# Kernel tuning notes

Measured on AMD Instinct MI355X. Metric: run time of the kernel, lower is better.

Reference implementation:

```python
import jax, jax.numpy as jnp
import numpy as np

N = 32768       # nodes
IN = 256        # in_channels
D = 128         # out_channels (per-head dim)
H = 4           # num_heads
M = 4           # num_reps (seeds per partition)
KP = 128        # number of partitions
S = N // KP     # partition size (equal-size partitions)
SCALE = float(np.sqrt(D))


def _linear_init(key, fan_in, fan_out):
    # torch nn.Linear default: U(-1/sqrt(fan_in), 1/sqrt(fan_in)) for W and b
    kw, kb = jax.random.split(key)
    bound = 1.0 / np.sqrt(fan_in)
    w = jax.random.uniform(kw, (fan_in, fan_out), jnp.float32, -bound, bound)
    b = jax.random.uniform(kb, (fan_out,), jnp.float32, -bound, bound)
    return w, b


def setup_inputs() -> dict:
    key = jax.random.key(0)
    k0, k1, k2, k3, k4 = jax.random.split(key, 5)
    x = jax.random.normal(k0, (N, IN), jnp.float32)
    # equal-size disjoint partitions: [KP, S] index array covering 0..N-1
    partition_indices = jnp.arange(N, dtype=jnp.int32).reshape(KP, S)
    Wq_w, Wq_b = _linear_init(k1, IN, H * D)
    Wk_w, Wk_b = _linear_init(k2, IN, H * D)
    Wv_w, Wv_b = _linear_init(k3, IN, H * D)
    pool_seeds = jax.random.normal(k4, (M, H, D), jnp.float32) * 0.02
    alpha_logit = jnp.float32(0.0)
    beta = jnp.float32(1.0)
    return {
        "x": x, "partition_indices": partition_indices,
        "Wq_w": Wq_w, "Wq_b": Wq_b, "Wk_w": Wk_w, "Wk_b": Wk_b,
        "Wv_w": Wv_w, "Wv_b": Wv_b, "pool_seeds": pool_seeds,
        "alpha_logit": alpha_logit, "beta": beta,
    }


def reference(x, partition_indices, Wq_w, Wq_b, Wk_w, Wk_b, Wv_w, Wv_b,
              pool_seeds, alpha_logit, beta):
    n = x.shape[0]
    Q = (x @ Wq_w + Wq_b).reshape(n, H, D)
    K = (x @ Wk_w + Wk_b).reshape(n, H, D)
    V = (x @ Wv_w + Wv_b).reshape(n, H, D)

    # gather per partition -> [KP, S, H, D]
    Qp = Q[partition_indices]
    Kp = K[partition_indices]
    Vp = V[partition_indices]

    # Fine: exact softmax attention within each partition
    attn_local = jnp.einsum('kphd,kqhd->khpq', Qp, Kp) / SCALE
    attn_local = jax.nn.softmax(attn_local, axis=-1)
    outp = jnp.einsum('khpq,kqhd->kphd', attn_local, Vp)  # [KP,S,H,D]
    # partitions are disjoint -> scatter-set back to node order
    out_local = jnp.zeros((n, H, D), x.dtype).at[partition_indices.reshape(-1)].set(
        outp.reshape(n, H, D))
    x_local = out_local.mean(axis=1)  # [N, D]

    # Coarse: learned seeds pool each partition
    pool_attn = jnp.einsum('mhd,kqhd->kmhq', pool_seeds, Kp) / SCALE
    pool_attn = jax.nn.softmax(pool_attn, axis=-1)
    reps_k = jnp.einsum('kmhq,kqhd->kmhd', pool_attn, Kp).reshape(KP * M, H, D)
    reps_v = jnp.einsum('kmhq,kqhd->kmhd', pool_attn, Vp).reshape(KP * M, H, D)

    # Global cross-attention: every node attends to all partition reps
    cross_attn = jnp.einsum('nhd,rhd->nhr', Q, reps_k) / SCALE
    cross_attn = jax.nn.softmax(cross_attn, axis=-1)
    out_global = jnp.einsum('nhr,rhd->nhd', cross_attn, reps_v)
    x_global = out_global.mean(axis=1)  # [N, D]

    x_self = V.mean(axis=1)
    alpha = jax.nn.sigmoid(alpha_logit)
    return alpha * x_local + (1.0 - alpha) * x_global + beta * x_self
```

## Files before the change

kernel.cpp:

```cpp
#include <hip/hip_runtime.h>
#include <hip/hip_bf16.h>


#define INV_SCALE 0.08838834764831845f
#define C2EXP 0.12751744f
#define DEFER_THR 90.50966799f

typedef __attribute__((ext_vector_type(8))) short bf16x8;
typedef __attribute__((ext_vector_type(4))) float floatx4;
typedef unsigned short ushort_t;
typedef unsigned int uint32;

#define OFF_Q    0ull
#define OFF_K    33554432ull
#define OFF_V    67108864ull
#define OFF_LOC  100663296ull
#define OFF_RPK  109051904ull
#define OFF_XC   110100480ull
#define OFF_WC   126877696ull
#define OFF_SCAL 127671296ull
#define OFF_FLAG 127671304ull
#define OFF_RVT  127672320ull
#define OFF_GLB  128196608ull

#define WC_WQ 0
#define WC_WK 131072
#define WC_WV 262144
#define WC_BQ 393216
#define WC_BK 393728
#define WC_BV 394240
#define WC_SEED 394752
#define WC_TOT 396800

static __device__ __forceinline__ float bflo(uint32 u) {
  return __uint_as_float(u << 16);
}
static __device__ __forceinline__ float bfhi(uint32 u) {
  return __uint_as_float(u & 0xffff0000u);
}
static __device__ __forceinline__ float bf2f(ushort_t u) {
  return __uint_as_float(((uint32)u) << 16);
}
static __device__ __forceinline__ ushort_t f2bf(float f) {
  uint32 x = __float_as_uint(f);
  uint32 r = x + 0x7fffu + ((x >> 16) & 1u);
  return (ushort_t)(r >> 16);
}
static __device__ __forceinline__ uint32 pack2bf(float a, float b) {
  return (uint32)f2bf(a) | ((uint32)f2bf(b) << 16);
}
static __device__ __forceinline__ uint32 cvtpk(float a, float b) {
  uint32 r;
  asm("v_cvt_pk_bf16_f32 %0, %1, %2" : "=v"(r) : "v"(a), "v"(b));
  return r;
}

static __device__ __forceinline__ void gl2lds16(const ushort_t* g, ushort_t* l) {
  __builtin_amdgcn_global_load_lds(
      (const __attribute__((address_space(1))) void*)g,
      (__attribute__((address_space(3))) void*)l, 16, 0, 0);
}

__global__ __launch_bounds__(64) void k_detect(const uint32* __restrict__ xw,
                                               const ushort_t* __restrict__ betaRaw,
                                               uint32* __restrict__ flags) {
  const int lane = threadIdx.x;
  const uint32 w = xw[lane * 137 + 3];
  const int e = (w >> 7) & 0xff;
  const unsigned long long b = __ballot(e >= 100 && e <= 140);
  if (lane == 0) {
    flags[0] = (__popcll(b) >= 48) ? 1u : 0u;
    flags[1] = (betaRaw[0] != 0) ? 1u : 0u;
  }
}

static __device__ __forceinline__ void conv8(const void* src, long j, int isB,
                                             ushort_t* dst) {
  if (isB) {
    *reinterpret_cast<uint4*>(dst) =
        *reinterpret_cast<const uint4*>(reinterpret_cast<const ushort_t*>(src) + j);
  } else {
    const float* f = reinterpret_cast<const float*>(src) + j;
    const float4 a = *reinterpret_cast<const float4*>(f);
    const float4 b = *reinterpret_cast<const float4*>(f + 4);
    uint4 o;
    o.x = pack2bf(a.x, a.y); o.y = pack2bf(a.z, a.w);
    o.z = pack2bf(b.x, b.y); o.w = pack2bf(b.z, b.w);
    *reinterpret_cast<uint4*>(dst) = o;
  }
}

__global__ __launch_bounds__(256) void k_convert(
    const void* __restrict__ x,
    const void* __restrict__ Wq, const void* __restrict__ bq,
    const void* __restrict__ Wk, const void* __restrict__ bk,
    const void* __restrict__ Wv, const void* __restrict__ bv,
    const void* __restrict__ seeds, const void* __restrict__ alpha,
    const void* __restrict__ beta,
    ushort_t* __restrict__ xc, ushort_t* __restrict__ wc,
    float* __restrict__ scal, const uint32* __restrict__ flags)
{
  const int isB = (int)flags[0];
  const long i8 = ((long)blockIdx.x * 256 + threadIdx.x) * 8;
  if (blockIdx.y == 0) {
    conv8(x, i8, isB, xc + i8);
  } else {
    if (i8 < WC_BQ) {
      const int sel = (int)(i8 >> 17);
      const long local = i8 & 131071;
      const int kk = (int)(local >> 9);
      const int nn = (int)(local & 511);
      const void* src = sel == 0 ? Wq : (sel == 1 ? Wk : Wv);
      ushort_t* dstW = wc + sel * 131072;
#pragma unroll
      for (int j = 0; j < 8; ++j) {
        ushort_t v;
        if (isB) v = reinterpret_cast<const ushort_t*>(src)[local + j];
        else     v = f2bf(reinterpret_cast<const float*>(src)[local + j]);
        dstW[(size_t)(nn + j) * 256 + kk] = v;
      }
    } else if (i8 < WC_TOT) {
      const void* src; long j;
      if (i8 < WC_BK)        { src = bq;    j = i8 - WC_BQ; }
      else if (i8 < WC_BV)   { src = bk;    j = i8 - WC_BK; }
      else if (i8 < WC_SEED) { src = bv;    j = i8 - WC_BV; }
      else                   { src = seeds; j = i8 - WC_SEED; }
      conv8(src, j, isB, wc + i8);
    }
    if (blockIdx.x == 0 && threadIdx.x == 0) {
      const int isBS = (int)flags[1];
      scal[0] = isBS ? bf2f(reinterpret_cast<const ushort_t*>(alpha)[0])
                     : reinterpret_cast<const float*>(alpha)[0];
      scal[1] = isBS ? bf2f(reinterpret_cast<const ushort_t*>(beta)[0])
                     : reinterpret_cast<const float*>(beta)[0];
    }
  }
}

__global__ __launch_bounds__(256) void k_qkv(
    const ushort_t* __restrict__ xc, const ushort_t* __restrict__ wc,
    ushort_t* __restrict__ Qb, ushort_t* __restrict__ Kb, ushort_t* __restrict__ Vb)
{
  const int m0 = blockIdx.x * 64;
  const int tid = threadIdx.x, lane = tid & 63, wv = tid >> 6;
  const int l16 = lane & 15, quad = lane >> 4;
  const int kswz = l16 & 7;

  __shared__ __align__(16) ushort_t Ws[2][64 * 256];

  bf16x8 af[8];
  {
    const ushort_t* xrow = xc + (size_t)(m0 + wv * 16 + l16) * 256 + quad * 8;
#pragma unroll
    for (int ks = 0; ks < 8; ++ks)
      af[ks] = *reinterpret_cast<const bf16x8*>(xrow + ks * 32);
  }

  const int wRL = lane >> 5;
  const int wCH = lane & 31;

#pragma unroll
  for (int j = 0; j < 8; ++j) {
    const int row = wv * 16 + j * 2 + wRL;
    gl2lds16(wc + (size_t)row * 256 + ((wCH ^ (row & 7)) << 3),
             &Ws[0][(wv * 16 + j * 2) * 256]);
  }
  __syncthreads();

  for (int t = 0; t < 24; ++t) {
    const int cur = t & 1;

    if (t < 23) {
      const int nb = cur ^ 1;
      const int tn = t + 1;
#pragma unroll
      for (int j = 0; j < 8; ++j) {
        const int row = wv * 16 + j * 2 + wRL;
        gl2lds16(wc + (size_t)(tn * 64 + row) * 256 + ((wCH ^ (row & 7)) << 3),
                 &Ws[nb][(wv * 16 + j * 2) * 256]);
      }
    }

    floatx4 acc[4] = {};
#pragma unroll
    for (int ks = 0; ks < 8; ++ks) {
      const int ac = ks * 4 + quad;
#pragma unroll
      for (int nt = 0; nt < 4; ++nt) {
        bf16x8 b = *reinterpret_cast<const bf16x8*>(
            &Ws[cur][(nt * 16 + l16) * 256 + ((ac ^ kswz) << 3)]);
        acc[nt] = __builtin_amdgcn_mfma_f32_16x16x32_bf16(af[ks], b, acc[nt], 0, 0, 0);
      }
    }

    const int sel = t >> 3, nc = t & 7;
    const ushort_t* bias = wc + WC_BQ + sel * 512;
    ushort_t* out = sel == 0 ? Qb : (sel == 1 ? Kb : Vb);
    const int n0 = nc * 64;
#pragma unroll
    for (int nt = 0; nt < 4; ++nt) {
      const int col = n0 + nt * 16 + l16;
      const float bf = bf2f(bias[col]);
#pragma unroll
      for (int r = 0; r < 4; ++r) {
        const int row = m0 + wv * 16 + quad * 4 + r;
        out[(size_t)row * 512 + col] = f2bf(acc[nt][r] + bf);
      }
    }

    __syncthreads();
  }
}

__global__ __launch_bounds__(256) void k_pool(
    const ushort_t* __restrict__ Kb, const ushort_t* __restrict__ Vb,
    const int* __restrict__ pidx_all, const ushort_t* __restrict__ wc,
    ushort_t* __restrict__ rpk, ushort_t* __restrict__ rvT)
{
  const int k = blockIdx.x, h = blockIdx.y;
  const int tid = threadIdx.x, lane = tid & 63, wv = tid >> 6;
  const int* pidx = pidx_all + k * 256;

  __shared__ __align__(16) ushort_t SB[128 * 256];
  const uint32* SBU = reinterpret_cast<const uint32*>(SB);

#pragma unroll
  for (int i = 0; i < 16; ++i) {
    const int e8 = tid + 256 * i;
    const int q = e8 >> 4, dc = (e8 & 15) * 8;
    uint4 kv = *reinterpret_cast<const uint4*>(Kb + (size_t)pidx[q] * 512 + h * 128 + dc);
    const ushort_t* ku = reinterpret_cast<const ushort_t*>(&kv);
    const int qp = q >> 1, qb = q & 1;
#pragma unroll
    for (int j = 0; j < 8; ++j) {
      const int d = dc + j;
      SB[d * 256 + (((qp ^ (d & 31)) << 1) | qb)] = ku[j];
    }
  }
  __syncthreads();

  float q00, q01, q10, q11;
  {
    const uint32* ssrc = reinterpret_cast<const uint32*>(wc + WC_SEED + (size_t)(wv * 4 + h) * 128);
    float s00 = 0.f, s01 = 0.f, s10 = 0.f, s11 = 0.f;
#pragma unroll 8
    for (int dc = 0; dc < 64; ++dc) {
      const uint32 qv = ssrc[dc];
      const float a0 = bflo(qv), a1 = bfhi(qv);
      const int d0 = dc * 2, d1 = d0 + 1;
      const int c0 = lane ^ (d0 & 31);
      const int c1 = lane ^ (d1 & 31);
      const uint32 u00 = SBU[d0 * 128 + c0];
      const uint32 u01 = SBU[d0 * 128 + c0 + 64];
      const uint32 u10 = SBU[d1 * 128 + c1];
      const uint32 u11 = SBU[d1 * 128 + c1 + 64];
      s00 += a0 * bflo(u00) + a1 * bflo(u10);
      s01 += a0 * bfhi(u00) + a1 * bfhi(u10);
      s10 += a0 * bflo(u01) + a1 * bflo(u11);
      s11 += a0 * bfhi(u01) + a1 * bfhi(u11);
    }
    s00 *= INV_SCALE; s01 *= INV_SCALE; s10 *= INV_SCALE; s11 *= INV_SCALE;
    float mx = fmaxf(fmaxf(s00, s01), fmaxf(s10, s11));
#pragma unroll
    for (int off = 32; off >= 1; off >>= 1) mx = fmaxf(mx, __shfl_xor(mx, off));
    const float e00 = __expf(s00 - mx), e01 = __expf(s01 - mx);
    const float e10 = __expf(s10 - mx), e11 = __expf(s11 - mx);
    float sm = e00 + e01 + e10 + e11;
#pragma unroll
    for (int off = 32; off >= 1; off >>= 1) sm += __shfl_xor(sm, off);
    const float inv = 1.0f / sm;
    q00 = e00 * inv; q01 = e01 * inv; q10 = e10 * inv; q11 = e11 * inv;
  }

  {
    float rk0 = 0.f, rk1 = 0.f;
    const int d0 = 2 * lane, d1 = 2 * lane + 1;
#pragma unroll 4
    for (int qp = 0; qp < 64; ++qp) {
      const float pa = __shfl(q00, qp), pb = __shfl(q01, qp);
      const float pc = __shfl(q10, qp), pd = __shfl(q11, qp);
      const int c0 = qp ^ (d0 & 31);
      const int c1 = qp ^ (d1 & 31);
      const uint32 u0  = SBU[d0 * 128 + c0];
      const uint32 u0b = SBU[d0 * 128 + c0 + 64];
      const uint32 u1  = SBU[d1 * 128 + c1];
      const uint32 u1b = SBU[d1 * 128 + c1 + 64];
      rk0 += pa * bflo(u0) + pb * bfhi(u0) + pc * bflo(u0b) + pd * bfhi(u0b);
      rk1 += pa * bflo(u1) + pb * bfhi(u1) + pc * bflo(u1b) + pd * bfhi(u1b);
    }
    reinterpret_cast<uint32*>(rpk + ((size_t)((k * 4 + wv) * 4 + h)) * 128)[lane] = pack2bf(rk0, rk1);
  }
  __syncthreads();

#pragma unroll
  for (int i = 0; i < 16; ++i) {
    const int e8 = tid + 256 * i;
    const int q = e8 >> 4, dc = (e8 & 15) * 8;
    uint4 vv = *reinterpret_cast<const uint4*>(Vb + (size_t)pidx[q] * 512 + h * 128 + dc);
    *reinterpret_cast<uint4*>(&SB[q * 128 + dc]) = vv;
  }
  __syncthreads();

  {
    float rv0 = 0.f, rv1 = 0.f;
#pragma unroll 4
    for (int qp = 0; qp < 64; ++qp) {
      const float pa = __shfl(q00, qp), pb = __shfl(q01, qp);
      const float pc = __shfl(q10, qp), pd = __shfl(q11, qp);
      const uint32 v00 = SBU[(2 * qp) * 64 + lane];
      const uint32 v01 = SBU[(2 * qp + 1) * 64 + lane];
      const uint32 v10 = SBU[(128 + 2 * qp) * 64 + lane];
      const uint32 v11 = SBU[(129 + 2 * qp) * 64 + lane];
      rv0 += pa * bflo(v00) + pb * bflo(v01) + pc * bflo(v10) + pd * bflo(v11);
      rv1 += pa * bfhi(v00) + pb * bfhi(v01) + pc * bfhi(v10) + pd * bfhi(v11);
    }
    const int rrep = k * 4 + wv;
    rvT[(size_t)(h * 128 + 2 * lane) * 512 + rrep]     = f2bf(rv0);
    rvT[(size_t)(h * 128 + 2 * lane + 1) * 512 + rrep] = f2bf(rv1);
  }
}

__global__ __launch_bounds__(256) void k_fine(
    const ushort_t* __restrict__ Qb, const ushort_t* __restrict__ Kb,
    const ushort_t* __restrict__ Vb, const int* __restrict__ pidx_all,
    ushort_t* __restrict__ locS)
{
  const int k = blockIdx.x, qg = blockIdx.y;
  const int tid = threadIdx.x, lane = tid & 63, wv = tid >> 6;
  const int l16 = lane & 15, quad = lane >> 4;
  const int* pidx = pidx_all + k * 256;

  __shared__ __align__(16) ushort_t BsK[2][64 * 128];
  __shared__ __align__(16) ushort_t SBV[128 * 64];
  __shared__ __align__(16) ushort_t Ps[4][16 * 72];

  const int qidx = pidx[qg * 64 + wv * 16 + l16];

  const int kRL = lane >> 4;
  const int kCH = lane & 15;
  const int kswz = l16 & 7;

  float accS[8][4];
#pragma unroll
  for (int nt = 0; nt < 8; ++nt)
#pragma unroll
    for (int r = 0; r < 4; ++r) accS[nt][r] = 0.f;

#pragma unroll
  for (int j = 0; j < 4; ++j) {
    const int row = wv * 16 + j * 4 + kRL;
    gl2lds16(Kb + (size_t)pidx[row] * 512 + ((kCH ^ (row & 7)) << 3),
             &BsK[0][(wv * 16 + j * 4) * 128]);
  }
  __syncthreads();

  bf16x8 qf[4];
  floatx4 O[8];
  float m_i = -3e38f, l_i = 0.f;

  for (int idx = 0; idx < 16; ++idx) {
    const int h = idx >> 2, c = idx & 3;
    const int cur = idx & 1;

    if (c == 0) {
      const ushort_t* qrow = Qb + (size_t)qidx * 512 + h * 128 + quad * 8;
#pragma unroll
      for (int ks = 0; ks < 4; ++ks)
        qf[ks] = *reinterpret_cast<const bf16x8*>(qrow + ks * 32);
#pragma unroll
      for (int nt = 0; nt < 8; ++nt) O[nt] = (floatx4){0.f, 0.f, 0.f, 0.f};
      m_i = -3e38f;
      l_i = 0.f;
    }

    if (idx < 15) {
      const int hn = (idx + 1) >> 2, cn = (idx + 1) & 3;
      const int nb = cur ^ 1;
#pragma unroll
      for (int j = 0; j < 4; ++j) {
        const int row = wv * 16 + j * 4 + kRL;
        gl2lds16(Kb + (size_t)pidx[cn * 64 + row] * 512 + hn * 128 +
                     ((kCH ^ (row & 7)) << 3),
                 &BsK[nb][(wv * 16 + j * 4) * 128]);
      }
    }

    floatx4 S[4] = {};
#pragma unroll
    for (int ks = 0; ks < 4; ++ks) {
      const int ac = ks * 4 + quad;
#pragma unroll
      for (int nt = 0; nt < 4; ++nt) {
        bf16x8 b = *reinterpret_cast<const bf16x8*>(
            &BsK[cur][(nt * 16 + l16) * 128 + ((ac ^ kswz) << 3)]);
        S[nt] = __builtin_amdgcn_mfma_f32_16x16x32_bf16(b, qf[ks], S[nt], 0, 0, 0);
      }
    }

    float cm;
    {
      const float m0 = fmaxf(fmaxf(S[0][0], S[0][1]), fmaxf(S[0][2], S[0][3]));
      const float m1 = fmaxf(fmaxf(S[1][0], S[1][1]), fmaxf(S[1][2], S[1][3]));
      const float m2 = fmaxf(fmaxf(S[2][0], S[2][1]), fmaxf(S[2][2], S[2][3]));
      const float m3 = fmaxf(fmaxf(S[3][0], S[3][1]), fmaxf(S[3][2], S[3][3]));
      cm = fmaxf(fmaxf(m0, m1), fmaxf(m2, m3));
      cm = fmaxf(cm, __shfl_xor(cm, 16));
      cm = fmaxf(cm, __shfl_xor(cm, 32));
    }
    if (!__all(cm <= m_i + DEFER_THR)) {
      const float mn = fmaxf(m_i, cm);
      const float sc = exp2f((m_i - mn) * C2EXP);
      m_i = mn;
      l_i *= sc;
      float scR[4];
#pragma unroll
      for (int r = 0; r < 4; ++r) scR[r] = __shfl(sc, quad * 4 + r);
#pragma unroll
      for (int nt = 0; nt < 8; ++nt)
#pragma unroll
        for (int r = 0; r < 4; ++r) O[nt][r] *= scR[r];
    }
    {
      const float mC = m_i * C2EXP;
      float ps = 0.f;
#pragma unroll
      for (int nt = 0; nt < 4; ++nt) {
        const float p0 = exp2f(S[nt][0] * C2EXP - mC);
        const float p1 = exp2f(S[nt][1] * C2EXP - mC);
        const float p2 = exp2f(S[nt][2] * C2EXP - mC);
        const float p3 = exp2f(S[nt][3] * C2EXP - mC);
        ps += (p0 + p1) + (p2 + p3);
        uint2 pk2 = make_uint2(pack2bf(p0, p1), pack2bf(p2, p3));
        *reinterpret_cast<uint2*>(&Ps[wv][l16 * 72 + nt * 16 + quad * 4]) = pk2;
      }
      ps += __shfl_xor(ps, 16);
      ps += __shfl_xor(ps, 32);
      l_i += ps;
    }

    __syncthreads();
#pragma unroll
    for (int i = 0; i < 4; ++i) {
      const int e = tid + 256 * i;
      const int key = e & 63, dc8 = (e >> 6) * 8;
      uint4 vv = *reinterpret_cast<const uint4*>(
          Vb + (size_t)pidx[c * 64 + key] * 512 + h * 128 + dc8);
      const ushort_t* u = reinterpret_cast<const ushort_t*>(&vv);
#pragma unroll
      for (int j = 0; j < 8; ++j) {
        const int d = dc8 + j;
        SBV[d * 64 + (((key >> 3) ^ j) << 3) + (key & 7)] = u[j];
      }
    }
    __syncthreads();

#pragma unroll
    for (int ks = 0; ks < 2; ++ks) {
      bf16x8 a = *reinterpret_cast<const bf16x8*>(&Ps[wv][l16 * 72 + ks * 32 + quad * 8]);
#pragma unroll
      for (int nt = 0; nt < 8; ++nt) {
        const int d = nt * 16 + l16;
        const int q8 = ks * 4 + quad;
        bf16x8 b = *reinterpret_cast<const bf16x8*>(
            &SBV[d * 64 + ((q8 ^ (d & 7)) << 3)]);
        O[nt] = __builtin_amdgcn_mfma_f32_16x16x32_bf16(a, b, O[nt], 0, 0, 0);
      }
    }

    if (c == 3) {
      float invR[4];
#pragma unroll
      for (int r = 0; r < 4; ++r) invR[r] = 1.0f / __shfl(l_i, quad * 4 + r);
#pragma unroll
      for (int nt = 0; nt < 8; ++nt)
#pragma unroll
        for (int r = 0; r < 4; ++r) accS[nt][r] += O[nt][r] * invR[r];
    }

    __syncthreads();
  }

#pragma unroll
  for (int r = 0; r < 4; ++r) {
    const int n = pidx[qg * 64 + wv * 16 + quad * 4 + r];
#pragma unroll
    for (int nt = 0; nt < 8; ++nt)
      locS[(size_t)n * 128 + nt * 16 + l16] = f2bf(accS[nt][r] * 0.25f);
  }
}

__global__ __launch_bounds__(256) void k_cross(
    const ushort_t* __restrict__ Qb, const ushort_t* __restrict__ rpk,
    const ushort_t* __restrict__ rvT, ushort_t* __restrict__ glb)
{
  const int h = blockIdx.y;
  const int n0 = blockIdx.x * 128;
  const int tid = threadIdx.x, lane = tid & 63, wv = tid >> 6;
  const int l16 = lane & 15, quad = lane >> 4;

  __shared__ __align__(16) ushort_t BsK[64 * 128];
  __shared__ __align__(16) ushort_t BsV[128 * 64];
  __shared__ __align__(16) ushort_t Ps[2][4][16 * 72];

  bf16x8 qf0[4], qf1[4];
  {
    const ushort_t* q0 =
        Qb + (size_t)(n0 + wv * 16 + l16) * 512 + h * 128 + quad * 8;
    const ushort_t* q1 = q0 + (size_t)64 * 512;
#pragma unroll
    for (int ks = 0; ks < 4; ++ks) {
      qf0[ks] = *reinterpret_cast<const bf16x8*>(q0 + ks * 32);
      qf1[ks] = *reinterpret_cast<const bf16x8*>(q1 + ks * 32);
    }
  }

  const int kRL = lane >> 4;
  const int kCH = lane & 15;
  const int vDL = lane >> 3;
  const int vCH = lane & 7;

  floatx4 O0[8] = {}, O1[8] = {};
  float m0_i = -3e38f, l0_i = 0.f;
  float m1_i = -3e38f, l1_i = 0.f;

  {
#pragma unroll
    for (int j = 0; j < 4; ++j) {
      const int row = wv * 16 + j * 4 + kRL;
      gl2lds16(rpk + (size_t)row * 512 + h * 128 + ((kCH ^ (row & 7)) << 3),
               &BsK[(wv * 16 + j * 4) * 128]);
      const int d = wv * 32 + j * 8 + vDL;
      gl2lds16(rvT + (size_t)(h * 128 + d) * 512 + ((vCH ^ (d & 7)) << 3),
               &BsV[(wv * 32 + j * 8) * 64]);
    }
  }
  __syncthreads();

  const int kswz = l16 & 7;

  for (int c = 0; c < 8; ++c) {
    floatx4 S0[4] = {}, S1[4] = {};
#pragma unroll
    for (int ks = 0; ks < 4; ++ks) {
      const int ac = ks * 4 + quad;
#pragma unroll
      for (int nt = 0; nt < 4; ++nt) {
        bf16x8 b = *reinterpret_cast<const bf16x8*>(
            &BsK[(nt * 16 + l16) * 128 + ((ac ^ kswz) << 3)]);
        S0[nt] = __builtin_amdgcn_mfma_f32_16x16x32_bf16(b, qf0[ks], S0[nt], 0, 0, 0);
        S1[nt] = __builtin_amdgcn_mfma_f32_16x16x32_bf16(b, qf1[ks], S1[nt], 0, 0, 0);
      }
    }

#pragma unroll
    for (int s = 0; s < 2; ++s) {
      floatx4* S      = (s == 0) ? S0 : S1;
      floatx4* O      = (s == 0) ? O0 : O1;
      float& m_i      = (s == 0) ? m0_i : m1_i;
      float& l_i      = (s == 0) ? l0_i : l1_i;

      float cm;
      {
        const float a0 = fmaxf(fmaxf(S[0][0], S[0][1]), fmaxf(S[0][2], S[0][3]));
        const float a1 = fmaxf(fmaxf(S[1][0], S[1][1]), fmaxf(S[1][2], S[1][3]));
        const float a2 = fmaxf(fmaxf(S[2][0], S[2][1]), fmaxf(S[2][2], S[2][3]));
        const float a3 = fmaxf(fmaxf(S[3][0], S[3][1]), fmaxf(S[3][2], S[3][3]));
        cm = fmaxf(fmaxf(a0, a1), fmaxf(a2, a3));
        cm = fmaxf(cm, __shfl_xor(cm, 16));
        cm = fmaxf(cm, __shfl_xor(cm, 32));
      }
      if (!__all(cm <= m_i + DEFER_THR)) {
        const float mn = fmaxf(m_i, cm);
        const float sc = exp2f((m_i - mn) * C2EXP);
        m_i = mn;
        l_i *= sc;
        float scR[4];
#pragma unroll
        for (int r = 0; r < 4; ++r) scR[r] = __shfl(sc, quad * 4 + r);
#pragma unroll
        for (int nt = 0; nt < 8; ++nt)
#pragma unroll
          for (int r = 0; r < 4; ++r) O[nt][r] *= scR[r];
      }
      {
        const float mC = m_i * C2EXP;
        float ps = 0.f;
#pragma unroll
        for (int nt = 0; nt < 4; ++nt) {
          const float p0 = exp2f(S[nt][0] * C2EXP - mC);
          const float p1 = exp2f(S[nt][1] * C2EXP - mC);
          const float p2 = exp2f(S[nt][2] * C2EXP - mC);
          const float p3 = exp2f(S[nt][3] * C2EXP - mC);
          ps += (p0 + p1) + (p2 + p3);
          uint2 pk2 = make_uint2(cvtpk(p0, p1), cvtpk(p2, p3));
          *reinterpret_cast<uint2*>(&Ps[s][wv][l16 * 72 + nt * 16 + quad * 4]) = pk2;
        }
        ps += __shfl_xor(ps, 16);
        ps += __shfl_xor(ps, 32);
        l_i += ps;
      }
    }

    __syncthreads();

    if (c < 7) {
      const int cn = c + 1;
#pragma unroll
      for (int j = 0; j < 4; ++j) {
        const int row = wv * 16 + j * 4 + kRL;
        gl2lds16(rpk + (size_t)(cn * 64 + row) * 512 + h * 128 +
                     ((kCH ^ (row & 7)) << 3),
                 &BsK[(wv * 16 + j * 4) * 128]);
      }
    }

#pragma unroll
    for (int ks = 0; ks < 2; ++ks) {
      bf16x8 a0 = *reinterpret_cast<const bf16x8*>(&Ps[0][wv][l16 * 72 + ks * 32 + quad * 8]);
      bf16x8 a1 = *reinterpret_cast<const bf16x8*>(&Ps[1][wv][l16 * 72 + ks * 32 + quad * 8]);
#pragma unroll
      for (int nt = 0; nt < 8; ++nt) {
        const int q8 = ks * 4 + quad;
        bf16x8 b = *reinterpret_cast<const bf16x8*>(
            &BsV[(nt * 16 + l16) * 64 + ((q8 ^ kswz) << 3)]);
        O0[nt] = __builtin_amdgcn_mfma_f32_16x16x32_bf16(a0, b, O0[nt], 0, 0, 0);
        O1[nt] = __builtin_amdgcn_mfma_f32_16x16x32_bf16(a1, b, O1[nt], 0, 0, 0);
      }
    }

    __syncthreads();

    if (c < 7) {
      const int cn = c + 1;
#pragma unroll
      for (int j = 0; j < 4; ++j) {
        const int d = wv * 32 + j * 8 + vDL;
        gl2lds16(rvT + (size_t)(h * 128 + d) * 512 + cn * 64 +
                     ((vCH ^ (d & 7)) << 3),
                 &BsV[(wv * 32 + j * 8) * 64]);
      }
    }
  }

#pragma unroll
  for (int s = 0; s < 2; ++s) {
    const floatx4* O = (s == 0) ? O0 : O1;
    const float l_i  = (s == 0) ? l0_i : l1_i;
    float invR[4];
#pragma unroll
    for (int r = 0; r < 4; ++r) invR[r] = 1.0f / __shfl(l_i, quad * 4 + r);
#pragma unroll
    for (int r = 0; r < 4; ++r) {
      const int n = n0 + s * 64 + wv * 16 + quad * 4 + r;
#pragma unroll
      for (int nt = 0; nt < 8; ++nt)
        glb[(size_t)n * 512 + h * 128 + nt * 16 + l16] = f2bf(O[nt][r] * invR[r]);
    }
  }
}

__global__ __launch_bounds__(256) void k_combine(
    const ushort_t* __restrict__ locS, const ushort_t* __restrict__ glb,
    const ushort_t* __restrict__ Vb, const float* __restrict__ scal,
    float* __restrict__ out)
{
  const int t = blockIdx.x * 256 + threadIdx.x;
  const int n = t >> 6, dp = t & 63;
  const float alpha = 1.0f / (1.0f + __expf(-scal[0]));
  const float beta = scal[1];
  const uint32 lv = reinterpret_cast<const uint32*>(locS)[(size_t)n * 64 + dp];
  float g0 = 0.f, g1 = 0.f, v0 = 0.f, v1 = 0.f;
#pragma unroll
  for (int hh = 0; hh < 4; ++hh) {
    const uint32 gv = *reinterpret_cast<const uint32*>(glb + (size_t)n * 512 + hh * 128 + 2 * dp);
    const uint32 vv = *reinterpret_cast<const uint32*>(Vb + (size_t)n * 512 + hh * 128 + 2 * dp);
    g0 += bflo(gv); g1 += bfhi(gv);
    v0 += bflo(vv); v1 += bfhi(vv);
  }
  const float r0 = alpha * bflo(lv) + (1.0f - alpha) * g0 * 0.25f + beta * v0 * 0.25f;
  const float r1 = alpha * bfhi(lv) + (1.0f - alpha) * g1 * 0.25f + beta * v1 * 0.25f;
  reinterpret_cast<float2*>(out)[(size_t)n * 64 + dp] = make_float2(r0, r1);
}

extern "C" void kernel_launch(void* const* d_in, const int* in_sizes, int n_in,
                              void* d_out, int out_size, void* d_ws, size_t ws_size,
                              hipStream_t stream) {
  const void* x     = d_in[0];
  const int*  pidx  = (const int*)d_in[1];
  const void* Wq    = d_in[2];
  const void* bq    = d_in[3];
  const void* Wk    = d_in[4];
  const void* bk    = d_in[5];
  const void* Wv    = d_in[6];
  const void* bv    = d_in[7];
  const void* seeds = d_in[8];
  const void* al    = d_in[9];
  const void* be    = d_in[10];

  char* ws = (char*)d_ws;
  ushort_t* Qb   = (ushort_t*)(ws + OFF_Q);
  ushort_t* Kb   = (ushort_t*)(ws + OFF_K);
  ushort_t* Vb   = (ushort_t*)(ws + OFF_V);
  ushort_t* locS = (ushort_t*)(ws + OFF_LOC);
  ushort_t* rpk  = (ushort_t*)(ws + OFF_RPK);
  ushort_t* xc   = (ushort_t*)(ws + OFF_XC);
  ushort_t* wc   = (ushort_t*)(ws + OFF_WC);
  float*    scal = (float*)   (ws + OFF_SCAL);
  uint32*   flags= (uint32*)  (ws + OFF_FLAG);
  ushort_t* rvT  = (ushort_t*)(ws + OFF_RVT);
  ushort_t* glb  = (ushort_t*)(ws + OFF_GLB);

  k_detect<<<1, 64, 0, stream>>>((const uint32*)x, (const ushort_t*)be, flags);
  k_convert<<<dim3(4096, 2), 256, 0, stream>>>(x, Wq, bq, Wk, bk, Wv, bv, seeds, al, be,
                                               xc, wc, scal, flags);
  k_qkv<<<512, 256, 0, stream>>>(xc, wc, Qb, Kb, Vb);
  k_pool<<<dim3(128, 4), 256, 0, stream>>>(Kb, Vb, pidx, wc, rpk, rvT);
  k_fine<<<dim3(128, 4), 256, 0, stream>>>(Qb, Kb, Vb, pidx, locS);
  k_cross<<<dim3(256, 4), 256, 0, stream>>>(Qb, rpk, rvT, glb);
  k_combine<<<8192, 256, 0, stream>>>(locS, glb, Vb, scal, (float*)d_out);
}
```

Measured before the change: 337.3 us.

## Merge fine and cross attention kernels into one interleaved launch

Fuses k_fine (512 blocks) and k_cross (1024 blocks) into a single k_attn kernel of 1536 blocks. Every third block runs the fine-attention path and the other two run cross-attention, and both share one LDS buffer. The cross path now double-buffers its K tile so the next chunk's load overlaps the current compute. The aim is to remove one launch and the tail gap between the two kernels so they co-schedule and balance across CUs. The cost is a larger unified LDS footprint, and register pressure is taken as the maximum of the two paths, which may lower occupancy.

```diff
diff --git a/kernel.cpp b/kernel.cpp
--- a/kernel.cpp
+++ b/kernel.cpp
@@ -320,252 +320,100 @@
   }
 }
 
-__global__ __launch_bounds__(256) void k_fine(
+__global__ __launch_bounds__(256) void k_attn(
     const ushort_t* __restrict__ Qb, const ushort_t* __restrict__ Kb,
     const ushort_t* __restrict__ Vb, const int* __restrict__ pidx_all,
-    ushort_t* __restrict__ locS)
+    const ushort_t* __restrict__ rpk, const ushort_t* __restrict__ rvT,
+    ushort_t* __restrict__ locS, ushort_t* __restrict__ glb)
 {
-  const int k = blockIdx.x, qg = blockIdx.y;
+  __shared__ __align__(16) ushort_t smem[33792];
+  ushort_t* BsK0 = smem;
+  ushort_t* BsK1 = smem + 8192;
+  ushort_t* SBV  = smem + 16384;
+  ushort_t* PsB  = smem + 24576;
+
+  const int gid = blockIdx.x;
+  const int t3 = gid % 3;
   const int tid = threadIdx.x, lane = tid & 63, wv = tid >> 6;
   const int l16 = lane & 15, quad = lane >> 4;
-  const int* pidx = pidx_all + k * 256;
-
-  __shared__ __align__(16) ushort_t BsK[2][64 * 128];
-  __shared__ __align__(16) ushort_t SBV[128 * 64];
-  __shared__ __align__(16) ushort_t Ps[4][16 * 72];
-
-  const int qidx = pidx[qg * 64 + wv * 16 + l16];
-
-  const int kRL = lane >> 4;
-  const int kCH = lane & 15;
   const int kswz = l16 & 7;
 
-  float accS[8][4];
-#pragma unroll
-  for (int nt = 0; nt < 8; ++nt)
-#pragma unroll
-    for (int r = 0; r < 4; ++r) accS[nt][r] = 0.f;
-
-#pragma unroll
-  for (int j = 0; j < 4; ++j) {
-    const int row = wv * 16 + j * 4 + kRL;
-    gl2lds16(Kb + (size_t)pidx[row] * 512 + ((kCH ^ (row & 7)) << 3),
-             &BsK[0][(wv * 16 + j * 4) * 128]);
-  }
-  __syncthreads();
-
-  bf16x8 qf[4];
-  floatx4 O[8];
-  float m_i = -3e38f, l_i = 0.f;
-
-  for (int idx = 0; idx < 16; ++idx) {
-    const int h = idx >> 2, c = idx & 3;
-    const int cur = idx & 1;
-
-    if (c == 0) {
-      const ushort_t* qrow = Qb + (size_t)qidx * 512 + h * 128 + quad * 8;
-#pragma unroll
-      for (int ks = 0; ks < 4; ++ks)
-        qf[ks] = *reinterpret_cast<const bf16x8*>(qrow + ks * 32);
-#pragma unroll
-      for (int nt = 0; nt < 8; ++nt) O[nt] = (floatx4){0.f, 0.f, 0.f, 0.f};
-      m_i = -3e38f;
-      l_i = 0.f;
-    }
-
-    if (idx < 15) {
-      const int hn = (idx + 1) >> 2, cn = (idx + 1) & 3;
-      const int nb = cur ^ 1;
-#pragma unroll
-      for (int j = 0; j < 4; ++j) {
-        const int row = wv * 16 + j * 4 + kRL;
-        gl2lds16(Kb + (size_t)pidx[cn * 64 + row] * 512 + hn * 128 +
-                     ((kCH ^ (row & 7)) << 3),
-                 &BsK[nb][(wv * 16 + j * 4) * 128]);
-      }
-    }
-
-    floatx4 S[4] = {};
-#pragma unroll
-    for (int ks = 0; ks < 4; ++ks) {
-      const int ac = ks * 4 + quad;
-#pragma unroll
-      for (int nt = 0; nt < 4; ++nt) {
-        bf16x8 b = *reinterpret_cast<const bf16x8*>(
-            &BsK[cur][(nt * 16 + l16) * 128 + ((ac ^ kswz) << 3)]);
-        S[nt] = __builtin_amdgcn_mfma_f32_16x16x32_bf16(b, qf[ks], S[nt], 0, 0, 0);
-      }
-    }
-
-    float cm;
-    {
-      const float m0 = fmaxf(fmaxf(S[0][0], S[0][1]), fmaxf(S[0][2], S[0][3]));
-      const float m1 = fmaxf(fmaxf(S[1][0], S[1][1]), fmaxf(S[1][2], S[1][3]));
-      const float m2 = fmaxf(fmaxf(S[2][0], S[2][1]), fmaxf(S[2][2], S[2][3]));
-      const float m3 = fmaxf(fmaxf(S[3][0], S[3][1]), fmaxf(S[3][2], S[3][3]));
-      cm = fmaxf(fmaxf(m0, m1), fmaxf(m2, m3));
-      cm = fmaxf(cm, __shfl_xor(cm, 16));
-      cm = fmaxf(cm, __shfl_xor(cm, 32));
-    }
-    if (!__all(cm <= m_i + DEFER_THR)) {
-      const float mn = fmaxf(m_i, cm);
-      const float sc = exp2f((m_i - mn) * C2EXP);
-      m_i = mn;
-      l_i *= sc;
-      float scR[4];
-#pragma unroll
-      for (int r = 0; r < 4; ++r) scR[r] = __shfl(sc, quad * 4 + r);
-#pragma unroll
-      for (int nt = 0; nt < 8; ++nt)
-#pragma unroll
-        for (int r = 0; r < 4; ++r) O[nt][r] *= scR[r];
-    }
-    {
-      const float mC = m_i * C2EXP;
-      float ps = 0.f;
-#pragma unroll
-      for (int nt = 0; nt < 4; ++nt) {
-        const float p0 = exp2f(S[nt][0] * C2EXP - mC);
-        const float p1 = exp2f(S[nt][1] * C2EXP - mC);
-        const float p2 = exp2f(S[nt][2] * C2EXP - mC);
-        const float p3 = exp2f(S[nt][3] * C2EXP - mC);
-        ps += (p0 + p1) + (p2 + p3);
-        uint2 pk2 = make_uint2(pack2bf(p0, p1), pack2bf(p2, p3));
-        *reinterpret_cast<uint2*>(&Ps[wv][l16 * 72 + nt * 16 + quad * 4]) = pk2;
-      }
-      ps += __shfl_xor(ps, 16);
-      ps += __shfl_xor(ps, 32);
-      l_i += ps;
-    }
-
-    __syncthreads();
-#pragma unroll
-    for (int i = 0; i < 4; ++i) {
-      const int e = tid + 256 * i;
-      const int key = e & 63, dc8 = (e >> 6) * 8;
-      uint4 vv = *reinterpret_cast<const uint4*>(
-          Vb + (size_t)pidx[c * 64 + key] * 512 + h * 128 + dc8);
-      const ushort_t* u = reinterpret_cast<const ushort_t*>(&vv);
-#pragma unroll
-      for (int j = 0; j < 8; ++j) {
-        const int d = dc8 + j;
-        SBV[d * 64 + (((key >> 3) ^ j) << 3) + (key & 7)] = u[j];
-      }
-    }
-    __syncthreads();
-
-#pragma unroll
-    for (int ks = 0; ks < 2; ++ks) {
-      bf16x8 a = *reinterpret_cast<const bf16x8*>(&Ps[wv][l16 * 72 + ks * 32 + quad * 8]);
-#pragma unroll
-      for (int nt = 0; nt < 8; ++nt) {
-        const int d = nt * 16 + l16;
-        const int q8 = ks * 4 + quad;
-        bf16x8 b = *reinterpret_cast<const bf16x8*>(
-            &SBV[d * 64 + ((q8 ^ (d & 7)) << 3)]);
-        O[nt] = __builtin_amdgcn_mfma_f32_16x16x32_bf16(a, b, O[nt], 0, 0, 0);
-      }
-    }
-
-    if (c == 3) {
-      float invR[4];
-#pragma unroll
-      for (int r = 0; r < 4; ++r) invR[r] = 1.0f / __shfl(l_i, quad * 4 + r);
-#pragma unroll
-      for (int nt = 0; nt < 8; ++nt)
-#pragma unroll
-        for (int r = 0; r < 4; ++r) accS[nt][r] += O[nt][r] * invR[r];
-    }
-
-    __syncthreads();
-  }
-
-#pragma unroll
-  for (int r = 0; r < 4; ++r) {
-    const int n = pidx[qg * 64 + wv * 16 + quad * 4 + r];
+  if (t3 == 0) {
+    const int fid = gid / 3;
+    const int k = fid >> 2, qg = fid & 3;
+    const int* pidx = pidx_all + k * 256;
+
+    const int qidx = pidx[qg * 64 + wv * 16 + l16];
+
+    const int kRL = lane >> 4;
+    const int kCH = lane & 15;
+
+    ushort_t* Psw = PsB + wv * (16 * 72);
+
+    float accS[8][4];
 #pragma unroll
     for (int nt = 0; nt < 8; ++nt)
-      locS[(size_t)n * 128 + nt * 16 + l16] = f2bf(accS[nt][r] * 0.25f);
-  }
-}
-
-__global__ __launch_bounds__(256) void k_cross(
-    const ushort_t* __restrict__ Qb, const ushort_t* __restrict__ rpk,
-    const ushort_t* __restrict__ rvT, ushort_t* __restrict__ glb)
-{
-  const int h = blockIdx.y;
-  const int n0 = blockIdx.x * 128;
-  const int tid = threadIdx.x, lane = tid & 63, wv = tid >> 6;
-  const int l16 = lane & 15, quad = lane >> 4;
-
-  __shared__ __align__(16) ushort_t BsK[64 * 128];
-  __shared__ __align__(16) ushort_t BsV[128 * 64];
-  __shared__ __align__(16) ushort_t Ps[2][4][16 * 72];
-
-  bf16x8 qf0[4], qf1[4];
-  {
-    const ushort_t* q0 =
-        Qb + (size_t)(n0 + wv * 16 + l16) * 512 + h * 128 + quad * 8;
-    const ushort_t* q1 = q0 + (size_t)64 * 512;
-#pragma unroll
-    for (int ks = 0; ks < 4; ++ks) {
-      qf0[ks] = *reinterpret_cast<const bf16x8*>(q0 + ks * 32);
-      qf1[ks] = *reinterpret_cast<const bf16x8*>(q1 + ks * 32);
-    }
-  }
-
-  const int kRL = lane >> 4;
-  const int kCH = lane & 15;
-  const int vDL = lane >> 3;
-  const int vCH = lane & 7;
-
-  floatx4 O0[8] = {}, O1[8] = {};
-  float m0_i = -3e38f, l0_i = 0.f;
-  float m1_i = -3e38f, l1_i = 0.f;
-
-  {
+#pragma unroll
+      for (int r = 0; r < 4; ++r) accS[nt][r] = 0.f;
+
 #pragma unroll
     for (int j = 0; j < 4; ++j) {
       const int row = wv * 16 + j * 4 + kRL;
-      gl2lds16(rpk + (size_t)row * 512 + h * 128 + ((kCH ^ (row & 7)) << 3),
-               &BsK[(wv * 16 + j * 4) * 128]);
-      const int d = wv * 32 + j * 8 + vDL;
-      gl2lds16(rvT + (size_t)(h * 128 + d) * 512 + ((vCH ^ (d & 7)) << 3),
-               &BsV[(wv * 32 + j * 8) * 64]);
-    }
-  }
-  __syncthreads();
-
-  const int kswz = l16 & 7;
-
-  for (int c = 0; c < 8; ++c) {
-    floatx4 S0[4] = {}, S1[4] = {};
-#pragma unroll
-    for (int ks = 0; ks < 4; ++ks) {
-      const int ac = ks * 4 + quad;
-#pragma unroll
-      for (int nt = 0; nt < 4; ++nt) {
-        bf16x8 b = *reinterpret_cast<const bf16x8*>(
-            &BsK[(nt * 16 + l16) * 128 + ((ac ^ kswz) << 3)]);
-        S0[nt] = __builtin_amdgcn_mfma_f32_16x16x32_bf16(b, qf0[ks], S0[nt], 0, 0, 0);
-        S1[nt] = __builtin_amdgcn_mfma_f32_16x16x32_bf16(b, qf1[ks], S1[nt], 0, 0, 0);
-      }
-    }
-
-#pragma unroll
-    for (int s = 0; s < 2; ++s) {
-      floatx4* S      = (s == 0) ? S0 : S1;
-      floatx4* O      = (s == 0) ? O0 : O1;
-      float& m_i      = (s == 0) ? m0_i : m1_i;
-      float& l_i      = (s == 0) ? l0_i : l1_i;
+      gl2lds16(Kb + (size_t)pidx[row] * 512 + ((kCH ^ (row & 7)) << 3),
+               &BsK0[(wv * 16 + j * 4) * 128]);
+    }
+    __syncthreads();
+
+    bf16x8 qf[4];
+    floatx4 O[8];
+    float m_i = -3e38f, l_i = 0.f;
+
+    for (int idx = 0; idx < 16; ++idx) {
+      const int h = idx >> 2, c = idx & 3;
+      ushort_t* Bcur = (idx & 1) ? BsK1 : BsK0;
+      ushort_t* Bnxt = (idx & 1) ? BsK0 : BsK1;
+
+      if (c == 0) {
+        const ushort_t* qrow = Qb + (size_t)qidx * 512 + h * 128 + quad * 8;
+#pragma unroll
+        for (int ks = 0; ks < 4; ++ks)
+          qf[ks] = *reinterpret_cast<const bf16x8*>(qrow + ks * 32);
+#pragma unroll
+        for (int nt = 0; nt < 8; ++nt) O[nt] = (floatx4){0.f, 0.f, 0.f, 0.f};
+        m_i = -3e38f;
+        l_i = 0.f;
+      }
+
+      if (idx < 15) {
+        const int hn = (idx + 1) >> 2, cn = (idx + 1) & 3;
+#pragma unroll
+        for (int j = 0; j < 4; ++j) {
+          const int row = wv * 16 + j * 4 + kRL;
+          gl2lds16(Kb + (size_t)pidx[cn * 64 + row] * 512 + hn * 128 +
+                       ((kCH ^ (row & 7)) << 3),
+                   &Bnxt[(wv * 16 + j * 4) * 128]);
+        }
+      }
+
+      floatx4 S[4] = {};
+#pragma unroll
+      for (int ks = 0; ks < 4; ++ks) {
+        const int ac = ks * 4 + quad;
+#pragma unroll
+        for (int nt = 0; nt < 4; ++nt) {
+          bf16x8 b = *reinterpret_cast<const bf16x8*>(
+              &Bcur[(nt * 16 + l16) * 128 + ((ac ^ kswz) << 3)]);
+          S[nt] = __builtin_amdgcn_mfma_f32_16x16x32_bf16(b, qf[ks], S[nt], 0, 0, 0);
+        }
+      }
 
       float cm;
       {
-        const float a0 = fmaxf(fmaxf(S[0][0], S[0][1]), fmaxf(S[0][2], S[0][3]));
-        const float a1 = fmaxf(fmaxf(S[1][0], S[1][1]), fmaxf(S[1][2], S[1][3]));
-        const float a2 = fmaxf(fmaxf(S[2][0], S[2][1]), fmaxf(S[2][2], S[2][3]));
-        const float a3 = fmaxf(fmaxf(S[3][0], S[3][1]), fmaxf(S[3][2], S[3][3]));
-        cm = fmaxf(fmaxf(a0, a1), fmaxf(a2, a3));
+        const float m0 = fmaxf(fmaxf(S[0][0], S[0][1]), fmaxf(S[0][2], S[0][3]));
+        const float m1 = fmaxf(fmaxf(S[1][0], S[1][1]), fmaxf(S[1][2], S[1][3]));
+        const float m2 = fmaxf(fmaxf(S[2][0], S[2][1]), fmaxf(S[2][2], S[2][3]));
+        const float m3 = fmaxf(fmaxf(S[3][0], S[3][1]), fmaxf(S[3][2], S[3][3]));
+        cm = fmaxf(fmaxf(m0, m1), fmaxf(m2, m3));
         cm = fmaxf(cm, __shfl_xor(cm, 16));
         cm = fmaxf(cm, __shfl_xor(cm, 32));
       }
@@ -592,69 +440,228 @@
           const float p2 = exp2f(S[nt][2] * C2EXP - mC);
           const float p3 = exp2f(S[nt][3] * C2EXP - mC);
           ps += (p0 + p1) + (p2 + p3);
-          uint2 pk2 = make_uint2(cvtpk(p0, p1), cvtpk(p2, p3));
-          *reinterpret_cast<uint2*>(&Ps[s][wv][l16 * 72 + nt * 16 + quad * 4]) = pk2;
+          uint2 pk2 = make_uint2(pack2bf(p0, p1), pack2bf(p2, p3));
+          *reinterpret_cast<uint2*>(&Psw[l16 * 72 + nt * 16 + quad * 4]) = pk2;
         }
         ps += __shfl_xor(ps, 16);
         ps += __shfl_xor(ps, 32);
         l_i += ps;
       }
-    }
-
-    __syncthreads();
-
-    if (c < 7) {
-      const int cn = c + 1;
+
+      __syncthreads();
+#pragma unroll
+      for (int i = 0; i < 4; ++i) {
+        const int e = tid + 256 * i;
+        const int key = e & 63, dc8 = (e >> 6) * 8;
+        uint4 vv = *reinterpret_cast<const uint4*>(
+            Vb + (size_t)pidx[c * 64 + key] * 512 + h * 128 + dc8);
+        const ushort_t* u = reinterpret_cast<const ushort_t*>(&vv);
+#pragma unroll
+        for (int j = 0; j < 8; ++j) {
+          const int d = dc8 + j;
+          SBV[d * 64 + (((key >> 3) ^ j) << 3) + (key & 7)] = u[j];
+        }
+      }
+      __syncthreads();
+
+#pragma unroll
+      for (int ks = 0; ks < 2; ++ks) {
+        bf16x8 a = *reinterpret_cast<const bf16x8*>(&Psw[l16 * 72 + ks * 32 + quad * 8]);
+#pragma unroll
+        for (int nt = 0; nt < 8; ++nt) {
+          const int d = nt * 16 + l16;
+          const int q8 = ks * 4 + quad;
+          bf16x8 b = *reinterpret_cast<const bf16x8*>(
+              &SBV[d * 64 + ((q8 ^ (d & 7)) << 3)]);
+          O[nt] = __builtin_amdgcn_mfma_f32_16x16x32_bf16(a, b, O[nt], 0, 0, 0);
+        }
+      }
+
+      if (c == 3) {
+        float invR[4];
+#pragma unroll
+        for (int r = 0; r < 4; ++r) invR[r] = 1.0f / __shfl(l_i, quad * 4 + r);
+#pragma unroll
+        for (int nt = 0; nt < 8; ++nt)
+#pragma unroll
+          for (int r = 0; r < 4; ++r) accS[nt][r] += O[nt][r] * invR[r];
+      }
+
+      __syncthreads();
+    }
+
+#pragma unroll
+    for (int r = 0; r < 4; ++r) {
+      const int n = pidx[qg * 64 + wv * 16 + quad * 4 + r];
+#pragma unroll
+      for (int nt = 0; nt < 8; ++nt)
+        locS[(size_t)n * 128 + nt * 16 + l16] = f2bf(accS[nt][r] * 0.25f);
+    }
+
+  } else {
+    const int cid = (gid / 3) * 2 + (t3 - 1);
+    const int h = cid & 3;
+    const int n0 = (cid >> 2) * 128;
+
+    ushort_t* Ps0 = PsB + wv * (16 * 72);
+    ushort_t* Ps1 = PsB + (4 + wv) * (16 * 72);
+
+    bf16x8 qf0[4], qf1[4];
+    {
+      const ushort_t* q0 =
+          Qb + (size_t)(n0 + wv * 16 + l16) * 512 + h * 128 + quad * 8;
+      const ushort_t* q1 = q0 + (size_t)64 * 512;
+#pragma unroll
+      for (int ks = 0; ks < 4; ++ks) {
+        qf0[ks] = *reinterpret_cast<const bf16x8*>(q0 + ks * 32);
+        qf1[ks] = *reinterpret_cast<const bf16x8*>(q1 + ks * 32);
+      }
+    }
+
+    const int kRL = lane >> 4;
+    const int kCH = lane & 15;
+    const int vDL = lane >> 3;
+    const int vCH = lane & 7;
+
+    floatx4 O0[8] = {}, O1[8] = {};
+    float m0_i = -3e38f, l0_i = 0.f;
+    float m1_i = -3e38f, l1_i = 0.f;
+
+    {
 #pragma unroll
       for (int j = 0; j < 4; ++j) {
         const int row = wv * 16 + j * 4 + kRL;
-        gl2lds16(rpk + (size_t)(cn * 64 + row) * 512 + h * 128 +
-                     ((kCH ^ (row & 7)) << 3),
-                 &BsK[(wv * 16 + j * 4) * 128]);
-      }
-    }
-
-#pragma unroll
-    for (int ks = 0; ks < 2; ++ks) {
-      bf16x8 a0 = *reinterpret_cast<const bf16x8*>(&Ps[0][wv][l16 * 72 + ks * 32 + quad * 8]);
-      bf16x8 a1 = *reinterpret_cast<const bf16x8*>(&Ps[1][wv][l16 * 72 + ks * 32 + quad * 8]);
-#pragma unroll
-      for (int nt = 0; nt < 8; ++nt) {
-        const int q8 = ks * 4 + quad;
-        bf16x8 b = *reinterpret_cast<const bf16x8*>(
-            &BsV[(nt * 16 + l16) * 64 + ((q8 ^ kswz) << 3)]);
-        O0[nt] = __builtin_amdgcn_mfma_f32_16x16x32_bf16(a0, b, O0[nt], 0, 0, 0);
-        O1[nt] = __builtin_amdgcn_mfma_f32_16x16x32_bf16(a1, b, O1[nt], 0, 0, 0);
-      }
-    }
-
+        gl2lds16(rpk + (size_t)row * 512 + h * 128 + ((kCH ^ (row & 7)) << 3),
+                 &BsK0[(wv * 16 + j * 4) * 128]);
+        const int d = wv * 32 + j * 8 + vDL;
+        gl2lds16(rvT + (size_t)(h * 128 + d) * 512 + ((vCH ^ (d & 7)) << 3),
+                 &SBV[(wv * 32 + j * 8) * 64]);
+      }
+    }
     __syncthreads();
 
-    if (c < 7) {
-      const int cn = c + 1;
-#pragma unroll
-      for (int j = 0; j < 4; ++j) {
-        const int d = wv * 32 + j * 8 + vDL;
-        gl2lds16(rvT + (size_t)(h * 128 + d) * 512 + cn * 64 +
-                     ((vCH ^ (d & 7)) << 3),
-                 &BsV[(wv * 32 + j * 8) * 64]);
-      }
-    }
-  }
-
-#pragma unroll
-  for (int s = 0; s < 2; ++s) {
-    const floatx4* O = (s == 0) ? O0 : O1;
-    const float l_i  = (s == 0) ? l0_i : l1_i;
-    float invR[4];
-#pragma unroll
-    for (int r = 0; r < 4; ++r) invR[r] = 1.0f / __shfl(l_i, quad * 4 + r);
-#pragma unroll
-    for (int r = 0; r < 4; ++r) {
-      const int n = n0 + s * 64 + wv * 16 + quad * 4 + r;
-#pragma unroll
-      for (int nt = 0; nt < 8; ++nt)
-        glb[(size_t)n * 512 + h * 128 + nt * 16 + l16] = f2bf(O[nt][r] * invR[r]);
+    for (int c = 0; c < 8; ++c) {
+      ushort_t* Bcur = (c & 1) ? BsK1 : BsK0;
+      ushort_t* Bnxt = (c & 1) ? BsK0 : BsK1;
+
+      if (c < 7) {
+        const int cn = c + 1;
+#pragma unroll
+        for (int j = 0; j < 4; ++j) {
+          const int row = wv * 16 + j * 4 + kRL;
+          gl2lds16(rpk + (size_t)(cn * 64 + row) * 512 + h * 128 +
+                       ((kCH ^ (row & 7)) << 3),
+                   &Bnxt[(wv * 16 + j * 4) * 128]);
+        }
+      }
+
+      floatx4 S0[4] = {}, S1[4] = {};
+#pragma unroll
+      for (int ks = 0; ks < 4; ++ks) {
+        const int ac = ks * 4 + quad;
+#pragma unroll
+        for (int nt = 0; nt < 4; ++nt) {
+          bf16x8 b = *reinterpret_cast<const bf16x8*>(
+              &Bcur[(nt * 16 + l16) * 128 + ((ac ^ kswz) << 3)]);
+          S0[nt] = __builtin_amdgcn_mfma_f32_16x16x32_bf16(b, qf0[ks], S0[nt], 0, 0, 0);
+          S1[nt] = __builtin_amdgcn_mfma_f32_16x16x32_bf16(b, qf1[ks], S1[nt], 0, 0, 0);
+        }
+      }
+
+#pragma unroll
+      for (int s = 0; s < 2; ++s) {
+        floatx4* S      = (s == 0) ? S0 : S1;
+        floatx4* O      = (s == 0) ? O0 : O1;
+        float& m_i      = (s == 0) ? m0_i : m1_i;
+        float& l_i      = (s == 0) ? l0_i : l1_i;
+        ushort_t* Psw   = (s == 0) ? Ps0 : Ps1;
+
+        float cm;
+        {
+          const float a0 = fmaxf(fmaxf(S[0][0], S[0][1]), fmaxf(S[0][2], S[0][3]));
+          const float a1 = fmaxf(fmaxf(S[1][0], S[1][1]), fmaxf(S[1][2], S[1][3]));
+          const float a2 = fmaxf(fmaxf(S[2][0], S[2][1]), fmaxf(S[2][2], S[2][3]));
+          const float a3 = fmaxf(fmaxf(S[3][0], S[3][1]), fmaxf(S[3][2], S[3][3]));
+          cm = fmaxf(fmaxf(a0, a1), fmaxf(a2, a3));
+          cm = fmaxf(cm, __shfl_xor(cm, 16));
+          cm = fmaxf(cm, __shfl_xor(cm, 32));
+        }
+        if (!__all(cm <= m_i + DEFER_THR)) {
+          const float mn = fmaxf(m_i, cm);
+          const float sc = exp2f((m_i - mn) * C2EXP);
+          m_i = mn;
+          l_i *= sc;
+          float scR[4];
+#pragma unroll
+          for (int r = 0; r < 4; ++r) scR[r] = __shfl(sc, quad * 4 + r);
+#pragma unroll
+          for (int nt = 0; nt < 8; ++nt)
+#pragma unroll
+            for (int r = 0; r < 4; ++r) O[nt][r] *= scR[r];
+        }
+        {
+          const float mC = m_i * C2EXP;
+          float ps = 0.f;
+#pragma unroll
+          for (int nt = 0; nt < 4; ++nt) {
+            const float p0 = exp2f(S[nt][0] * C2EXP - mC);
+            const float p1 = exp2f(S[nt][1] * C2EXP - mC);
+            const float p2 = exp2f(S[nt][2] * C2EXP - mC);
+            const float p3 = exp2f(S[nt][3] * C2EXP - mC);
+            ps += (p0 + p1) + (p2 + p3);
+            uint2 pk2 = make_uint2(cvtpk(p0, p1), cvtpk(p2, p3));
+            *reinterpret_cast<uint2*>(&Psw[l16 * 72 + nt * 16 + quad * 4]) = pk2;
+          }
+          ps += __shfl_xor(ps, 16);
+          ps += __shfl_xor(ps, 32);
+          l_i += ps;
+        }
+      }
+
+      __syncthreads();
+
+#pragma unroll
+      for (int ks = 0; ks < 2; ++ks) {
+        bf16x8 a0 = *reinterpret_cast<const bf16x8*>(&Ps0[l16 * 72 + ks * 32 + quad * 8]);
+        bf16x8 a1 = *reinterpret_cast<const bf16x8*>(&Ps1[l16 * 72 + ks * 32 + quad * 8]);
+#pragma unroll
+        for (int nt = 0; nt < 8; ++nt) {
+          const int q8 = ks * 4 + quad;
+          bf16x8 b = *reinterpret_cast<const bf16x8*>(
+              &SBV[(nt * 16 + l16) * 64 + ((q8 ^ kswz) << 3)]);
+          O0[nt] = __builtin_amdgcn_mfma_f32_16x16x32_bf16(a0, b, O0[nt], 0, 0, 0);
+          O1[nt] = __builtin_amdgcn_mfma_f32_16x16x32_bf16(a1, b, O1[nt], 0, 0, 0);
+        }
+      }
+
+      __syncthreads();
+
+      if (c < 7) {
+        const int cn = c + 1;
+#pragma unroll
+        for (int j = 0; j < 4; ++j) {
+          const int d = wv * 32 + j * 8 + vDL;
+          gl2lds16(rvT + (size_t)(h * 128 + d) * 512 + cn * 64 +
+                       ((vCH ^ (d & 7)) << 3),
+                   &SBV[(wv * 32 + j * 8) * 64]);
+        }
+      }
+    }
+
+#pragma unroll
+    for (int s = 0; s < 2; ++s) {
+      const floatx4* O = (s == 0) ? O0 : O1;
+      const float l_i  = (s == 0) ? l0_i : l1_i;
+      float invR[4];
+#pragma unroll
+      for (int r = 0; r < 4; ++r) invR[r] = 1.0f / __shfl(l_i, quad * 4 + r);
+#pragma unroll
+      for (int r = 0; r < 4; ++r) {
+        const int n = n0 + s * 64 + wv * 16 + quad * 4 + r;
+#pragma unroll
+        for (int nt = 0; nt < 8; ++nt)
+          glb[(size_t)n * 512 + h * 128 + nt * 16 + l16] = f2bf(O[nt][r] * invR[r]);
+      }
     }
   }
 }
@@ -715,7 +722,6 @@
                                                xc, wc, scal, flags);
   k_qkv<<<512, 256, 0, stream>>>(xc, wc, Qb, Kb, Vb);
   k_pool<<<dim3(128, 4), 256, 0, stream>>>(Kb, Vb, pidx, wc, rpk, rvT);
-  k_fine<<<dim3(128, 4), 256, 0, stream>>>(Qb, Kb, Vb, pidx, locS);
-  k_cross<<<dim3(256, 4), 256, 0, stream>>>(Qb, rpk, rvT, glb);
+  k_attn<<<1536, 256, 0, stream>>>(Qb, Kb, Vb, pidx, rpk, rvT, locS, glb);
   k_combine<<<8192, 256, 0, stream>>>(locS, glb, Vb, scal, (float*)d_out);
 }
```

Result: slower. 388.7 us (+15.2%).
